# Performance work log

Hardware: AMD Instinct MI355X
Metric: run time of the kernel (lower is better)

The kernel has to match this reference:

```python
import jax, jax.numpy as jnp
import numpy as np

B, L, F, E, D, N_OUT, FC = 2048, 100, 64, 256, 256, 3, 128


def _lstm_cell(x, h, c, Wi, Wh, b):
    gates = x @ Wi + h @ Wh + b  # (B, 4H)
    i, f, g, o = jnp.split(gates, 4, axis=-1)
    c_new = jax.nn.sigmoid(f) * c + jax.nn.sigmoid(i) * jnp.tanh(g)
    h_new = jax.nn.sigmoid(o) * jnp.tanh(c_new)
    return h_new, c_new


def setup_inputs() -> dict:
    key = jax.random.key(0)
    ks = jax.random.split(key, 12)
    s = 0.05
    return {
        "x": jax.random.normal(ks[0], (B, L, F), jnp.float32),
        # encoder input-attention (shared across timesteps, as in [layer]*look_back)
        "Wa": jax.random.normal(ks[1], (F + E, F), jnp.float32) * s,
        "ba": jnp.zeros((F,), jnp.float32),
        # encoder LSTM cell
        "Wi": jax.random.normal(ks[2], (F, 4 * E), jnp.float32) * s,
        "Wh": jax.random.normal(ks[3], (E, 4 * E), jnp.float32) * s,
        "be": jnp.zeros((4 * E,), jnp.float32),
        # decoder temporal attention
        "Wd": jax.random.normal(ks[4], (E + D, D), jnp.float32) * s,
        "bd": jnp.zeros((D,), jnp.float32),
        "Wl": jax.random.normal(ks[5], (D, 1), jnp.float32) * s,
        "bl": jnp.zeros((1,), jnp.float32),
        # decoder LSTM cell
        "Wdi": jax.random.normal(ks[6], (E, 4 * D), jnp.float32) * s,
        "Wdh": jax.random.normal(ks[7], (D, 4 * D), jnp.float32) * s,
        "bdec": jnp.zeros((4 * D,), jnp.float32),
        # output head: tanh(D->FC) then tanh(FC->1)
        "Wf": jax.random.normal(ks[8], (D, FC), jnp.float32) * s,
        "bf": jnp.zeros((FC,), jnp.float32),
        "Wo": jax.random.normal(ks[9], (FC, 1), jnp.float32) * s,
        "bo": jnp.zeros((1,), jnp.float32),
    }


def reference(x, Wa, ba, Wi, Wh, be, Wd, bd, Wl, bl, Wdi, Wdh, bdec, Wf, bf, Wo, bo):
    # ---------- encoder: per-timestep input attention + LSTM cell ----------
    x_t = jnp.transpose(x, (1, 0, 2))  # (L, B, F)

    def enc_step(carry, xt):
        h, c = carry
        energies = jnp.tanh(jnp.concatenate([xt, h], axis=1) @ Wa + ba)  # (B, F)
        a = jax.nn.softmax(energies, axis=1)
        enc_in = a * xt  # attended input (B, F)
        h, c = _lstm_cell(enc_in, h, c, Wi, Wh, be)
        return (h, c), h

    h0 = jnp.zeros((B, E), x.dtype)
    c0 = jnp.zeros((B, E), x.dtype)
    _, enc_out = jax.lax.scan(enc_step, (h0, c0), x_t)  # (L, B, E)

    # ---------- decoder: temporal attention over encoder states + LSTM ----------
    h_d = jnp.zeros((B, D), x.dtype)
    c_d = jnp.zeros((B, D), x.dtype)
    outs = []
    for _ in range(N_OUT):  # small fixed output horizon
        con = jnp.broadcast_to(h_d[None, :, :], (L, B, D))
        en = jnp.tanh(jnp.concatenate([enc_out, con], axis=2) @ Wd + bd)  # (L, B, D)
        scores = en @ Wl + bl  # (L, B, 1)
        alpha = jax.nn.softmax(scores, axis=0)  # over time
        ctx = jnp.sum(alpha * enc_out, axis=0)  # (B, E)
        h_d, c_d = _lstm_cell(ctx, h_d, c_d, Wdi, Wdh, bdec)
        fc = jnp.tanh(h_d @ Wf + bf)  # (B, FC)
        outs.append(jnp.tanh(fc @ Wo + bo))  # (B, 1)
    return jnp.concatenate(outs, axis=1)  # (B, n_output)
```

## Files before the change

### kernel.cpp

```cpp
#include <hip/hip_runtime.h>
#include <math.h>

#define BB 2048
#define LL 100
#define FF 64
#define EE 256
#define DD 256
#define NOUT 3

#define COMP(v, i) ((i) == 0 ? (v).x : (i) == 1 ? (v).y : (i) == 2 ? (v).z : (v).w)

typedef unsigned short u16;
typedef unsigned int u32;
typedef __attribute__((ext_vector_type(8))) __bf16 bf16x8;
typedef __attribute__((ext_vector_type(4))) float f32x4;
typedef __attribute__((ext_vector_type(2))) float f32x2;

#define MFMA_(A, B, C) __builtin_amdgcn_mfma_f32_16x16x32_bf16((A), (B), (C), 0, 0, 0)

__device__ __forceinline__ float sigmoidf_(float x) {
    return 1.0f / (1.0f + expf(-x));
}
__device__ __forceinline__ float tanhf_(float x) {
    return 1.0f - 2.0f / (1.0f + expf(2.0f * x));
}
__device__ __forceinline__ u16 f2b_(float f) {
    u32 u = __float_as_uint(f);
    u = (u + 0x7FFFu + ((u >> 16) & 1u)) >> 16;
    return (u16)u;
}
__device__ __forceinline__ float b2f_(u16 b) {
    return __uint_as_float(((u32)b) << 16);
}
__device__ __forceinline__ u32 pack2_(float a, float b) {
    return (u32)f2b_(a) | ((u32)f2b_(b) << 16);
}
__device__ __forceinline__ f32x4 splat4(float b) {
    f32x4 v; v[0] = b; v[1] = b; v[2] = b; v[3] = b; return v;
}
__device__ __forceinline__ void split8(const float* v, uint4& H, uint4& L) {
    u16 h[8], lo[8];
    #pragma unroll
    for (int e = 0; e < 8; ++e) {
        h[e]  = f2b_(v[e]);
        lo[e] = f2b_(v[e] - b2f_(h[e]));
    }
    H = make_uint4((u32)h[0]  | ((u32)h[1]  << 16), (u32)h[2]  | ((u32)h[3]  << 16),
                   (u32)h[4]  | ((u32)h[5]  << 16), (u32)h[6]  | ((u32)h[7]  << 16));
    L = make_uint4((u32)lo[0] | ((u32)lo[1] << 16), (u32)lo[2] | ((u32)lo[3] << 16),
                   (u32)lo[4] | ((u32)lo[5] << 16), (u32)lo[6] | ((u32)lo[7] << 16));
}

#define AF(mt, kt, p, ln) (((((mt) * 10 + (kt)) * 2 + (p)) * 64 + (ln)) * 8)
#define AF2(mt, kt, p, ln) (((((mt) * 8 + (kt)) * 2 + (p)) * 64 + (ln)) * 8)

__global__ __launch_bounds__(64) void w_prep(
    const float* __restrict__ Wi, const float* __restrict__ Wh,
    const float* __restrict__ Wa, u16* __restrict__ wp)
{
    const int bid = blockIdx.x;
    const int l   = threadIdx.x;
    const int isA = (bid >= 640);
    const int b2  = isA ? bid - 640 : bid;
    const int nt  = b2 / 10, kt = b2 - nt * 10;
    const int col = nt * 16 + (l & 15);

    float v[8];
    #pragma unroll
    for (int e = 0; e < 8; ++e) {
        const int k = kt * 32 + ((l >> 4) << 3) + e;
        v[e] = isA ? Wa[(size_t)k * 64 + col]
                   : (k < 64 ? Wi[(size_t)k * 1024 + col]
                             : Wh[(size_t)(k - 64) * 1024 + col]);
    }
    uint4 H, L;
    split8(v, H, L);
    *(uint4*)&wp[(size_t)bid * 1024 + (size_t)l * 8]       = H;
    *(uint4*)&wp[(size_t)bid * 1024 + 512 + (size_t)l * 8] = L;
}

__global__ __launch_bounds__(64) void w_prep2(
    const float* __restrict__ Wd, u16* __restrict__ wp)
{
    const int bid = blockIdx.x;
    const int l   = threadIdx.x;
    const int nt  = bid >> 3, kt = bid & 7;
    const int col = nt * 16 + (l & 15);
    float v[8];
    #pragma unroll
    for (int e = 0; e < 8; ++e) {
        const int k = kt * 32 + ((l >> 4) << 3) + e;
        v[e] = Wd[(size_t)k * 256 + col];
    }
    uint4 H, L;
    split8(v, H, L);
    u16* tp = wp + (size_t)(680 + bid) * 1024;
    *(uint4*)&tp[(size_t)l * 8]       = H;
    *(uint4*)&tp[512 + (size_t)l * 8] = L;
}

__global__ __launch_bounds__(1024) void enc_mfma4(
    const float* __restrict__ x,
    const float* __restrict__ ba, const float* __restrict__ be,
    const u16* __restrict__ wp,
    float* __restrict__ enc_out,
    float* __restrict__ hbuf,
    u32* __restrict__ flags)
{
    __shared__ u16   aFrag[20480];
    __shared__ float x_s[32 * 68];
    __shared__ float e_s[32 * 68];
    __shared__ float gate_s[4][32][66];

    const int bid = blockIdx.x;
    const int g   = (bid & 7) | ((bid >> 5) << 3);
    const int p   = (bid >> 3) & 3;
    const int row0 = g * 32;
    const int tid = threadIdx.x;
    const int l   = tid & 63;
    const int w   = tid >> 6;

    for (int v = tid; v < 20480 / 2; v += 1024) ((u32*)aFrag)[v] = 0u;

    const int ntW = (w >> 2) * 16 + p * 4 + (w & 3);
    uint4 BhR[10], BlR[10];
    #pragma unroll
    for (int kt = 0; kt < 10; ++kt) {
        BhR[kt] = *(const uint4*)&wp[(size_t)(ntW * 10 + kt) * 1024 + (size_t)l * 8];
        BlR[kt] = *(const uint4*)&wp[(size_t)(ntW * 10 + kt) * 1024 + 512 + (size_t)l * 8];
    }

    const float be_r = be[(size_t)ntW * 16 + (l & 15)];
    const float ba_r = (w < 8) ? ba[(w & 3) * 16 + (l & 15)] : 0.f;

    float c_state[2] = {0.f, 0.f};

    __syncthreads();

    for (int t = 0; t < LL; ++t) {
        if (tid < 256) {
            const int kt2 = tid >> 7;
            const int mt  = (tid >> 6) & 1;
            const int l2  = tid & 63;
            const int row2 = mt * 16 + (l2 & 15);
            const int f0   = kt2 * 32 + ((l2 >> 4) << 3);
            const float* xp = x + (size_t)(row0 + row2) * (LL * FF) + (size_t)t * FF + f0;
            float4 xa = *(const float4*)xp;
            float4 xb = *(const float4*)(xp + 4);
            float v[8] = {xa.x, xa.y, xa.z, xa.w, xb.x, xb.y, xb.z, xb.w};
            uint4 H, L;
            split8(v, H, L);
            *(uint4*)&aFrag[AF(mt, kt2, 0, l2)] = H;
            *(uint4*)&aFrag[AF(mt, kt2, 1, l2)] = L;
            *(float4*)&x_s[row2 * 68 + f0]     = xa;
            *(float4*)&x_s[row2 * 68 + f0 + 4] = xb;
        } else if (t > 0) {
            const u32 target = 4u * (u32)t;
            int guard = 0;
            while (__hip_atomic_load(&flags[g * 32], __ATOMIC_RELAXED,
                                     __HIP_MEMORY_SCOPE_AGENT) < target) {
                __builtin_amdgcn_s_sleep(1);
                if (++guard > 4000000) break;
            }
            const int v   = tid - 256;
            const int prl = v >> 8;
            const int vv  = v & 255;
            const int row = vv >> 3;
            const int i8  = vv & 7;
            const int ugp = (p + 1 + prl) & 3;
            const int u8  = ugp * 64 + i8 * 8;
            const float* hp_g = hbuf + ((size_t)((t - 1) & 1) * BB + row0 + row) * 256 + u8;
            f32x4 a4, b4;
            asm volatile("global_load_dwordx4 %0, %2, off sc0 sc1\n\t"
                         "global_load_dwordx4 %1, %3, off sc0 sc1\n\t"
                         "s_waitcnt vmcnt(0)"
                         : "=v"(a4), "=v"(b4)
                         : "v"(hp_g), "v"(hp_g + 4) : "memory");
            float v8[8] = {a4[0], a4[1], a4[2], a4[3], b4[0], b4[1], b4[2], b4[3]};
            uint4 H, L;
            split8(v8, H, L);
            const int mt = row >> 4, rowT = row & 15;
            const int kt_h = 2 + (u8 >> 5);
            const int g2   = (u8 & 31) >> 3;
            const int ln   = rowT + (g2 << 4);
            *(uint4*)&aFrag[AF(mt, kt_h, 0, ln)] = H;
            *(uint4*)&aFrag[AF(mt, kt_h, 1, ln)] = L;
        }
        __syncthreads();

        if (w < 8) {
            const int mt  = w >> 2;
            const int nta = w & 3;
            f32x4 ea = splat4(ba_r);
            #pragma unroll
            for (int kt = 0; kt < 10; ++kt) {
                bf16x8 Ah = *(const bf16x8*)&aFrag[AF(mt, kt, 0, l)];
                bf16x8 Al = *(const bf16x8*)&aFrag[AF(mt, kt, 1, l)];
                const size_t o = (size_t)(640 + nta * 10 + kt) * 1024 + (size_t)l * 8;
                bf16x8 Bh = *(const bf16x8*)&wp[o];
                bf16x8 Bl = *(const bf16x8*)&wp[o + 512];
                ea = MFMA_(Ah, Bh, ea);
                ea = MFMA_(Al, Bh, ea);
                ea = MFMA_(Ah, Bl, ea);
            }
            const int colA = nta * 16 + (l & 15);
            #pragma unroll
            for (int r = 0; r < 4; ++r) {
                const int rowT = ((l >> 4) << 2) + r;
                e_s[(mt * 16 + rowT) * 68 + colA] = tanhf_(ea[r]);
            }
        }
        __syncthreads();

        if (tid < 512) {
            const int row2 = tid >> 4;
            const int c4   = (tid & 15) * 4;
            float4 ev = *(const float4*)&e_s[row2 * 68 + c4];
            float m = fmaxf(fmaxf(ev.x, ev.y), fmaxf(ev.z, ev.w));
            #pragma unroll
            for (int msk = 8; msk >= 1; msk >>= 1) m = fmaxf(m, __shfl_xor(m, msk, 64));
            float4 ex;
            ex.x = expf(ev.x - m); ex.y = expf(ev.y - m);
            ex.z = expf(ev.z - m); ex.w = expf(ev.w - m);
            float s = ex.x + ex.y + ex.z + ex.w;
            #pragma unroll
            for (int msk = 8; msk >= 1; msk >>= 1) s += __shfl_xor(s, msk, 64);
            const float inv = 1.f / s;
            float4 xv = *(const float4*)&x_s[row2 * 68 + c4];
            float ein[4] = { ex.x * inv * xv.x, ex.y * inv * xv.y,
                             ex.z * inv * xv.z, ex.w * inv * xv.w };
            const int mt   = row2 >> 4;
            const int rowT = row2 & 15;
            const int kt   = c4 >> 5;
            const int g2   = (c4 & 31) >> 3;
            const int e0   = c4 & 7;
            const int ln   = rowT + (g2 << 4);
            ushort4 h4, l4;
            #pragma unroll
            for (int e = 0; e < 4; ++e) {
                u16 hh = f2b_(ein[e]);
                u16 ll = f2b_(ein[e] - b2f_(hh));
                if (e == 0) { h4.x = hh; l4.x = ll; } else if (e == 1) { h4.y = hh; l4.y = ll; }
                else if (e == 2) { h4.z = hh; l4.z = ll; } else { h4.w = hh; l4.w = ll; }
            }
            *(ushort4*)&aFrag[AF(mt, kt, 0, ln) + e0] = h4;
            *(ushort4*)&aFrag[AF(mt, kt, 1, ln) + e0] = l4;
        }
        __syncthreads();

        f32x4 acc0 = splat4(be_r), acc1 = splat4(be_r);
        #pragma unroll
        for (int kt = 0; kt < 10; ++kt) {
            bf16x8 Ah0 = *(const bf16x8*)&aFrag[AF(0, kt, 0, l)];
            bf16x8 Al0 = *(const bf16x8*)&aFrag[AF(0, kt, 1, l)];
            bf16x8 Ah1 = *(const bf16x8*)&aFrag[AF(1, kt, 0, l)];
            bf16x8 Al1 = *(const bf16x8*)&aFrag[AF(1, kt, 1, l)];
            bf16x8 Bh  = __builtin_bit_cast(bf16x8, BhR[kt]);
            bf16x8 Bl  = __builtin_bit_cast(bf16x8, BlR[kt]);
            acc0 = MFMA_(Ah0, Bh, acc0);
            acc1 = MFMA_(Ah1, Bh, acc1);
            acc0 = MFMA_(Al0, Bh, acc0);
            acc1 = MFMA_(Al1, Bh, acc1);
            acc0 = MFMA_(Ah0, Bl, acc0);
            acc1 = MFMA_(Ah1, Bl, acc1);
        }
        {
            const int gate = w >> 2;
            const int ulb  = (w & 3) * 16 + (l & 15);
            #pragma unroll
            for (int r = 0; r < 4; ++r) {
                const int rT = ((l >> 4) << 2) + r;
                gate_s[gate][rT][ulb]      = acc0[r];
                gate_s[gate][16 + rT][ulb] = acc1[r];
            }
        }
        __syncthreads();

        {
            const int row = tid >> 5;
            const int q2  = (tid & 31) * 2;
            float gi0 = gate_s[0][row][q2], gi1 = gate_s[0][row][q2 + 1];
            float gf0 = gate_s[1][row][q2], gf1 = gate_s[1][row][q2 + 1];
            float gg0 = gate_s[2][row][q2], gg1 = gate_s[2][row][q2 + 1];
            float go0 = gate_s[3][row][q2], go1 = gate_s[3][row][q2 + 1];
            float cv0 = sigmoidf_(gf0) * c_state[0] + sigmoidf_(gi0) * tanhf_(gg0);
            float cv1 = sigmoidf_(gf1) * c_state[1] + sigmoidf_(gi1) * tanhf_(gg1);
            c_state[0] = cv0; c_state[1] = cv1;
            float hv0 = sigmoidf_(go0) * tanhf_(cv0);
            float hv1 = sigmoidf_(go1) * tanhf_(cv1);
            const int u_g = p * 64 + q2;
            *(float2*)&enc_out[((size_t)t * BB + row0 + row) * 256 + u_g]
                = make_float2(hv0, hv1);
            float* hp_g = hbuf + ((size_t)(t & 1) * BB + row0 + row) * 256 + u_g;
            f32x2 hv2; hv2[0] = hv0; hv2[1] = hv1;
            asm volatile("global_store_dwordx2 %0, %1, off sc0 sc1"
                         :: "v"(hp_g), "v"(hv2) : "memory");
            const int mt = row >> 4, rowT = row & 15;
            const int kt_h = 2 + (u_g >> 5);
            const int g2   = (u_g & 31) >> 3;
            const int ln   = rowT + (g2 << 4);
            const int e    = u_g & 7;
            ((u32*)aFrag)[(AF(mt, kt_h, 0, ln) + e) >> 1] = pack2_(hv0, hv1);
            u16 h0 = f2b_(hv0), h1 = f2b_(hv1);
            ((u32*)aFrag)[(AF(mt, kt_h, 1, ln) + e) >> 1] =
                (u32)f2b_(hv0 - b2f_(h0)) | ((u32)f2b_(hv1 - b2f_(h1)) << 16);
        }
        asm volatile("s_waitcnt vmcnt(0)" ::: "memory");
        __syncthreads();
        if (tid == 0)
            __hip_atomic_fetch_add(&flags[g * 32], 1u, __ATOMIC_RELEASE,
                                   __HIP_MEMORY_SCOPE_AGENT);
    }
}

__global__ __launch_bounds__(256) void gemm_ep_mfma(
    const float* __restrict__ A, const u16* __restrict__ wp,
    float* __restrict__ C)
{
    __shared__ u16   aF[2 * 8 * 2 * 64 * 8];
    __shared__ float c_s[32 * 260];
    const int m0  = blockIdx.x * 32;
    const int tid = threadIdx.x;
    const int l   = tid & 63;
    const int w   = tid >> 6;

    for (int s = tid; s < 1024; s += 256) {
        const int mt = s >> 9, kt = (s >> 6) & 7, l2 = s & 63;
        const int row2 = mt * 16 + (l2 & 15);
        const int k0   = kt * 32 + ((l2 >> 4) << 3);
        const float* ap = A + (size_t)(m0 + row2) * 256 + k0;
        float4 xa = *(const float4*)ap;
        float4 xb = *(const float4*)(ap + 4);
        float v[8] = {xa.x, xa.y, xa.z, xa.w, xb.x, xb.y, xb.z, xb.w};
        uint4 H, L;
        split8(v, H, L);
        *(uint4*)&aF[AF2(mt, kt, 0, l2)] = H;
        *(uint4*)&aF[AF2(mt, kt, 1, l2)] = L;
    }
    __syncthreads();

    f32x4 acc[2][4];
    #pragma unroll
    for (int mt = 0; mt < 2; ++mt)
        #pragma unroll
        for (int j = 0; j < 4; ++j) acc[mt][j] = splat4(0.f);

    #pragma unroll
    for (int kt = 0; kt < 8; ++kt) {
        bf16x8 Ah0 = *(const bf16x8*)&aF[AF2(0, kt, 0, l)];
        bf16x8 Al0 = *(const bf16x8*)&aF[AF2(0, kt, 1, l)];
        bf16x8 Ah1 = *(const bf16x8*)&aF[AF2(1, kt, 0, l)];
        bf16x8 Al1 = *(const bf16x8*)&aF[AF2(1, kt, 1, l)];
        #pragma unroll
        for (int j = 0; j < 4; ++j) {
            const int nt = w * 4 + j;
            const u16* bt = wp + (size_t)(680 + nt * 8 + kt) * 1024 + (size_t)l * 8;
            bf16x8 Bh = *(const bf16x8*)bt;
            bf16x8 Bl = *(const bf16x8*)(bt + 512);
            acc[0][j] = MFMA_(Ah0, Bh, acc[0][j]);
            acc[1][j] = MFMA_(Ah1, Bh, acc[1][j]);
            acc[0][j] = MFMA_(Al0, Bh, acc[0][j]);
            acc[1][j] = MFMA_(Al1, Bh, acc[1][j]);
            acc[0][j] = MFMA_(Ah0, Bl, acc[0][j]);
            acc[1][j] = MFMA_(Ah1, Bl, acc[1][j]);
        }
    }

    #pragma unroll
    for (int mt = 0; mt < 2; ++mt)
        #pragma unroll
        for (int j = 0; j < 4; ++j) {
            const int col = (w * 4 + j) * 16 + (l & 15);
            #pragma unroll
            for (int r = 0; r < 4; ++r) {
                const int row = mt * 16 + ((l >> 4) << 2) + r;
                c_s[row * 260 + col] = acc[mt][j][r];
            }
        }
    __syncthreads();
    for (int v = tid; v < 32 * 64; v += 256) {
        const int row = v >> 6, c4 = (v & 63) << 2;
        *(float4*)&C[(size_t)(m0 + row) * 256 + c4] = *(const float4*)&c_s[row * 260 + c4];
    }
}

__global__ __launch_bounds__(256) void gemm_nk256(
    const float* __restrict__ A, const float* __restrict__ W,
    const float* __restrict__ bias, float* __restrict__ C, int skip_gemm)
{
    __shared__ float a_s[32 * 256];
    const int m0   = blockIdx.x * 32;
    const int tid  = threadIdx.x;
    const int lane = tid & 63;
    const int rg   = tid >> 6;
    const int n0   = lane * 4;

    float4 bias4 = make_float4(0.f, 0.f, 0.f, 0.f);
    if (bias) bias4 = *(const float4*)&bias[n0];

    if (skip_gemm) {
        #pragma unroll
        for (int r = 0; r < 8; ++r)
            *(float4*)&C[(size_t)(m0 + rg * 8 + r) * 256 + n0] = bias4;
        return;
    }

    for (int v = tid; v < 32 * 64; v += 256)
        ((float4*)a_s)[v] = ((const float4*)(A + (size_t)m0 * 256))[v];
    __syncthreads();

    float4 acc[8];
    #pragma unroll
    for (int r = 0; r < 8; ++r) acc[r] = bias4;

    #pragma unroll 2
    for (int k = 0; k < 256; k += 4) {
        float4 wv[4];
        #pragma unroll
        for (int kk = 0; kk < 4; ++kk)
            wv[kk] = *(const float4*)&W[(size_t)(k + kk) * 256 + n0];
        float4 av[8];
        #pragma unroll
        for (int r = 0; r < 8; ++r)
            av[r] = *(const float4*)&a_s[(rg * 8 + r) * 256 + k];
        #pragma unroll
        for (int kk = 0; kk < 4; ++kk) {
            #pragma unroll
            for (int r = 0; r < 8; ++r) {
                float e = COMP(av[r], kk);
                acc[r].x += e * wv[kk].x; acc[r].y += e * wv[kk].y;
                acc[r].z += e * wv[kk].z; acc[r].w += e * wv[kk].w;
            }
        }
    }
    #pragma unroll
    for (int r = 0; r < 8; ++r)
        *(float4*)&C[(size_t)(m0 + rg * 8 + r) * 256 + n0] = acc[r];
}

__global__ __launch_bounds__(256) void pack_ep(
    float* A, const float* __restrict__ W, u16* epOut, int packed)
{
    __shared__ float a_s[32 * 256];
    const int m0   = blockIdx.x * 32;
    const int tid  = threadIdx.x;
    const int lane = tid & 63;
    const int rg   = tid >> 6;
    const int n0   = lane * 4;

    for (int v = tid; v < 32 * 64; v += 256)
        ((float4*)a_s)[v] = ((const float4*)(A + (size_t)m0 * 256))[v];
    __syncthreads();

    float4 acc[8];
    #pragma unroll
    for (int r = 0; r < 8; ++r) acc[r] = make_float4(0.f, 0.f, 0.f, 0.f);

    #pragma unroll 2
// ... 219 lines not shown
                acc[r].x += av.w * w3.x; acc[r].y += av.w * w3.y;
                acc[r].z += av.w * w3.z; acc[r].w += av.w * w3.w;
            }
        }
    } else if (!first) {
        const float* wP = Wdh + c0;
        #pragma unroll 2
        for (int ch = 0; ch < 64; ++ch) {
            const int k0 = ch * 4;
            float4 w0 = *(const float4*)&wP[(size_t)(k0 + 0) * 1024];
            float4 w1 = *(const float4*)&wP[(size_t)(k0 + 1) * 1024];
            float4 w2 = *(const float4*)&wP[(size_t)(k0 + 2) * 1024];
            float4 w3 = *(const float4*)&wP[(size_t)(k0 + 3) * 1024];
            #pragma unroll
            for (int r = 0; r < 8; ++r) {
                float4 av = *(const float4*)&hd_s[r * 256 + k0];
                acc[r].x += av.x * w0.x; acc[r].y += av.x * w0.y;
                acc[r].z += av.x * w0.z; acc[r].w += av.x * w0.w;
                acc[r].x += av.y * w1.x; acc[r].y += av.y * w1.y;
                acc[r].z += av.y * w1.z; acc[r].w += av.y * w1.w;
                acc[r].x += av.z * w2.x; acc[r].y += av.z * w2.y;
                acc[r].z += av.z * w2.z; acc[r].w += av.z * w2.w;
                acc[r].x += av.w * w3.x; acc[r].y += av.w * w3.y;
                acc[r].z += av.w * w3.z; acc[r].w += av.w * w3.w;
            }
        }
    }
    #pragma unroll
    for (int r = 0; r < 8; ++r)
        *(float4*)&gate_s[half][r * 1024 + c0] = acc[r];
    __syncthreads();

    {
        const float* g0 = &gate_s[0][w * 1024 + lane * 4];
        const float* g1 = &gate_s[1][w * 1024 + lane * 4];
        float4 giA = *(const float4*)&g0[0],   giB = *(const float4*)&g1[0];
        float4 gfA = *(const float4*)&g0[256], gfB = *(const float4*)&g1[256];
        float4 ggA = *(const float4*)&g0[512], ggB = *(const float4*)&g1[512];
        float4 goA = *(const float4*)&g0[768], goB = *(const float4*)&g1[768];
        size_t ci = (size_t)(row0 + w) * 256 + lane * 4;
        float4 c4 = first ? make_float4(0.f, 0.f, 0.f, 0.f)
                          : *(const float4*)&c_st[ci];
        float cc[4] = { c4.x, c4.y, c4.z, c4.w };
        float gi[4] = { giA.x + giB.x, giA.y + giB.y, giA.z + giB.z, giA.w + giB.w };
        float gf[4] = { gfA.x + gfB.x, gfA.y + gfB.y, gfA.z + gfB.z, gfA.w + gfB.w };
        float gg[4] = { ggA.x + ggB.x, ggA.y + ggB.y, ggA.z + ggB.z, ggA.w + ggB.w };
        float go[4] = { goA.x + goB.x, goA.y + goB.y, goA.z + goB.z, goA.w + goB.w };
        float4 cn, hn;
        #pragma unroll
        for (int uu = 0; uu < 4; ++uu) {
            float cv = sigmoidf_(gf[uu]) * cc[uu] + sigmoidf_(gi[uu]) * tanhf_(gg[uu]);
            float hv = sigmoidf_(go[uu]) * tanhf_(cv);
            if (uu == 0) { cn.x = cv; hn.x = hv; } else if (uu == 1) { cn.y = cv; hn.y = hv; }
            else if (uu == 2) { cn.z = cv; hn.z = hv; } else { cn.w = cv; hn.w = hv; }
        }
        *(float4*)&c_st[ci] = cn;
        *(float4*)&hd[ci]   = hn;
    }
}

__global__ __launch_bounds__(256) void head_k(
    const float* __restrict__ hd, const float* __restrict__ Wf,
    const float* __restrict__ bf, const float* __restrict__ Wo,
    const float* __restrict__ bo, float* __restrict__ out, int step)
{
    __shared__ float hd_s[16 * 256];
    __shared__ float fc_s[16 * 128];
    const int b0  = blockIdx.x * 16;
    const int tid = threadIdx.x;
    {
        const float4* hg = (const float4*)(hd + (size_t)b0 * 256);
        for (int i = tid; i < 1024; i += 256) ((float4*)hd_s)[i] = hg[i];
    }
    __syncthreads();
    {
        const int f = tid & 127, rg = tid >> 7;
        float acc[8];
        float bfv = bf[f];
        #pragma unroll
        for (int rr = 0; rr < 8; ++rr) acc[rr] = bfv;
        const float* wp = Wf + f;
        #pragma unroll 2
        for (int k = 0; k < 256; ++k) {
            float wv = wp[k * 128];
            #pragma unroll
            for (int rr = 0; rr < 8; ++rr) acc[rr] += hd_s[(rg * 8 + rr) * 256 + k] * wv;
        }
        for (int rr = 0; rr < 8; ++rr) fc_s[(rg * 8 + rr) * 128 + f] = tanhf_(acc[rr]);
    }
    __syncthreads();
    {
        const int lane = tid & 63, w = tid >> 6;
        const float bov = bo[0];
        #pragma unroll
        for (int rr = 0; rr < 4; ++rr) {
            int r = w * 4 + rr;
            float p = fc_s[r * 128 + lane] * Wo[lane] + fc_s[r * 128 + 64 + lane] * Wo[64 + lane];
            #pragma unroll
            for (int msk = 32; msk >= 1; msk >>= 1) p += __shfl_xor(p, msk, 64);
            if (lane == 0) out[(size_t)(b0 + r) * NOUT + step] = tanhf_(p + bov);
        }
    }
}

extern "C" void kernel_launch(void* const* d_in, const int* in_sizes, int n_in,
                              void* d_out, int out_size, void* d_ws, size_t ws_size,
                              hipStream_t stream)
{
    const float* x    = (const float*)d_in[0];
    const float* Wa   = (const float*)d_in[1];
    const float* ba   = (const float*)d_in[2];
    const float* Wi   = (const float*)d_in[3];
    const float* Wh   = (const float*)d_in[4];
    const float* be   = (const float*)d_in[5];
    const float* Wd   = (const float*)d_in[6];
    const float* bd   = (const float*)d_in[7];
    const float* Wl   = (const float*)d_in[8];
    const float* bl   = (const float*)d_in[9];
    const float* Wdi  = (const float*)d_in[10];
    const float* Wdh  = (const float*)d_in[11];
    const float* bdec = (const float*)d_in[12];
    const float* Wf   = (const float*)d_in[13];
    const float* bf   = (const float*)d_in[14];
    const float* Wo   = (const float*)d_in[15];
    const float* bo   = (const float*)d_in[16];
    float* out = (float*)d_out;

    const size_t f_enc    = (size_t)LL * BB * EE;
    const size_t f_state  = (size_t)BB * EE;
    const size_t f_scores = (size_t)LL * BB;
    const size_t need3 = (f_enc + 3 * f_state + f_scores) * sizeof(float);
    const size_t need2 = need3 + f_enc * sizeof(u16);
    const size_t need1 = need3 + f_enc * sizeof(float);

    float* ws      = (float*)d_ws;
    float* enc_out = ws;
    float* hd      = enc_out + f_enc;
    float* c_d     = hd + f_state;
    float* ctx     = c_d + f_state;
    float* scores  = ctx + f_state;
    float* ep32    = scores + f_scores;
    u16*   ep16    = (u16*)(scores + f_scores);
    float* hp      = ctx;
    u16*   wprep   = (u16*)ctx;
    float* hbuf    = hd;
    u32*   flags   = (u32*)scores;

    if (ws_size < need3) return;
    const int tier = (ws_size >= need1) ? 1 : (ws_size >= need2) ? 2 : 3;

    hipMemsetAsync(flags, 0, 64 * 32 * sizeof(u32), stream);
    w_prep<<<680, 64, 0, stream>>>(Wi, Wh, Wa, wprep);
    w_prep2<<<128, 64, 0, stream>>>(Wd, wprep);
    enc_mfma4<<<256, 1024, 0, stream>>>(x, ba, be, wprep, enc_out, hbuf, flags);

    if (tier == 1)
        gemm_ep_mfma<<<(LL * BB) / 32, 256, 0, stream>>>(enc_out, wprep, ep32);
    else
        pack_ep<<<(LL * BB) / 32, 256, 0, stream>>>(
            enc_out, Wd, ep16, tier == 3 ? 1 : 0);

    for (int s = 0; s < NOUT; ++s) {
        gemm_nk256<<<BB / 32, 256, 0, stream>>>(
            hd, Wd + 256 * 256, bd, hp, s == 0);
        if (tier == 1)
            scores_ep_f32<<<dim3(BB / 8, 5), 256, 0, stream>>>(ep32, hp, Wl, scores);
        else if (tier == 2)
            scores_ep_b16<<<dim3(BB / 8, 5), 256, 0, stream>>>(ep16, hp, Wl, scores, 256, 0);
        else
            scores_ep_b16<<<dim3(BB / 8, 5), 256, 0, stream>>>(
                (const u16*)enc_out, hp, Wl, scores, 512, 256);
        if (tier == 3)
            softmax_ctx_b16<<<BB / 8, 256, 0, stream>>>(scores, (const u16*)enc_out, ctx);
        else
            softmax_ctx<<<BB / 8, 256, 0, stream>>>(scores, enc_out, ctx);
        dec_step<<<BB / 8, 512, 0, stream>>>(ctx, Wdi, Wdh, bdec, hd, c_d, s == 0);
        head_k<<<BB / 16, 256, 0, stream>>>(hd, Wf, bf, Wo, bo, out, s);
    }
}
```

Baseline: 2.754 ms.

## Halve encoder block to 512 threads with two gate tiles per wave

The persistent encoder kernel drops from 1024 to 512 threads per block. Each wave now holds register-resident weights for two gate column tiles and issues twice as many MFMAs per step, and the attention GEMM has each wave cover both row tiles. Flag polling moves to a single thread followed by a barrier, and each remaining thread loads three hidden-state chunks. The LSTM elementwise stage handles four units per thread with wider stores. The aim is to cut barrier and cross-block sync cost. The trade is more register pressure, fewer waves to hide latency, and an extra barrier per timestep.

```diff
diff --git a/kernel.cpp b/kernel.cpp
--- a/kernel.cpp
+++ b/kernel.cpp
@@ -14,7 +14,6 @@
 typedef unsigned int u32;
 typedef __attribute__((ext_vector_type(8))) __bf16 bf16x8;
 typedef __attribute__((ext_vector_type(4))) float f32x4;
-typedef __attribute__((ext_vector_type(2))) float f32x2;
 
 #define MFMA_(A, B, C) __builtin_amdgcn_mfma_f32_16x16x32_bf16((A), (B), (C), 0, 0, 0)
 
@@ -99,7 +98,7 @@
     *(uint4*)&tp[512 + (size_t)l * 8] = L;
 }
 
-__global__ __launch_bounds__(1024) void enc_mfma4(
+__global__ __launch_bounds__(512, 2) void enc_mfma4(
     const float* __restrict__ x,
     const float* __restrict__ ba, const float* __restrict__ be,
     const u16* __restrict__ wp,
@@ -120,20 +119,26 @@
     const int l   = tid & 63;
     const int w   = tid >> 6;
 
-    for (int v = tid; v < 20480 / 2; v += 1024) ((u32*)aFrag)[v] = 0u;
-
-    const int ntW = (w >> 2) * 16 + p * 4 + (w & 3);
-    uint4 BhR[10], BlR[10];
+    for (int v = tid; v < 20480 / 2; v += 512) ((u32*)aFrag)[v] = 0u;
+
+    const int ln0 = 2 * w, ln1 = 2 * w + 1;
+    const int ntW0 = (ln0 >> 2) * 16 + p * 4 + (ln0 & 3);
+    const int ntW1 = (ln1 >> 2) * 16 + p * 4 + (ln1 & 3);
+    uint4 BH0[10], BL0[10], BH1[10], BL1[10];
     #pragma unroll
     for (int kt = 0; kt < 10; ++kt) {
-        BhR[kt] = *(const uint4*)&wp[(size_t)(ntW * 10 + kt) * 1024 + (size_t)l * 8];
-        BlR[kt] = *(const uint4*)&wp[(size_t)(ntW * 10 + kt) * 1024 + 512 + (size_t)l * 8];
-    }
-
-    const float be_r = be[(size_t)ntW * 16 + (l & 15)];
-    const float ba_r = (w < 8) ? ba[(w & 3) * 16 + (l & 15)] : 0.f;
-
-    float c_state[2] = {0.f, 0.f};
+        const size_t o0 = (size_t)(ntW0 * 10 + kt) * 1024 + (size_t)l * 8;
+        const size_t o1 = (size_t)(ntW1 * 10 + kt) * 1024 + (size_t)l * 8;
+        BH0[kt] = *(const uint4*)&wp[o0];
+        BL0[kt] = *(const uint4*)&wp[o0 + 512];
+        BH1[kt] = *(const uint4*)&wp[o1];
+        BL1[kt] = *(const uint4*)&wp[o1 + 512];
+    }
+    const float be_r0 = be[(size_t)ntW0 * 16 + (l & 15)];
+    const float be_r1 = be[(size_t)ntW1 * 16 + (l & 15)];
+    const float ba_r  = (w < 4) ? ba[w * 16 + (l & 15)] : 0.f;
+
+    float c_state[4] = {0.f, 0.f, 0.f, 0.f};
 
     __syncthreads();
 
@@ -154,65 +159,86 @@
             *(uint4*)&aFrag[AF(mt, kt2, 1, l2)] = L;
             *(float4*)&x_s[row2 * 68 + f0]     = xa;
             *(float4*)&x_s[row2 * 68 + f0 + 4] = xb;
-        } else if (t > 0) {
+        } else if (tid == 511 && t > 0) {
             const u32 target = 4u * (u32)t;
             int guard = 0;
             while (__hip_atomic_load(&flags[g * 32], __ATOMIC_RELAXED,
                                      __HIP_MEMORY_SCOPE_AGENT) < target) {
                 __builtin_amdgcn_s_sleep(1);
-                if (++guard > 4000000) break;
-            }
-            const int v   = tid - 256;
-            const int prl = v >> 8;
-            const int vv  = v & 255;
-            const int row = vv >> 3;
-            const int i8  = vv & 7;
-            const int ugp = (p + 1 + prl) & 3;
-            const int u8  = ugp * 64 + i8 * 8;
-            const float* hp_g = hbuf + ((size_t)((t - 1) & 1) * BB + row0 + row) * 256 + u8;
-            f32x4 a4, b4;
-            asm volatile("global_load_dwordx4 %0, %2, off sc0 sc1\n\t"
-                         "global_load_dwordx4 %1, %3, off sc0 sc1\n\t"
-                         "s_waitcnt vmcnt(0)"
-                         : "=v"(a4), "=v"(b4)
-                         : "v"(hp_g), "v"(hp_g + 4) : "memory");
-            float v8[8] = {a4[0], a4[1], a4[2], a4[3], b4[0], b4[1], b4[2], b4[3]};
-            uint4 H, L;
-            split8(v8, H, L);
+                if (++guard > 2000000) break;
+            }
+        }
+        __syncthreads();
+
+        if (t > 0 && tid >= 256) {
+            const int base = tid - 256;
+            const int row  = base >> 3;
+            const int i8   = base & 7;
+            const float* hb = hbuf + ((size_t)((t - 1) & 1) * BB + row0 + row) * 256;
+            const int u8a = (((p + 1) & 3) * 64) + i8 * 8;
+            const int u8b = (((p + 2) & 3) * 64) + i8 * 8;
+            const int u8c = (((p + 3) & 3) * 64) + i8 * 8;
+            f32x4 d0, d1, d2, d3, d4, d5;
+            asm volatile(
+                "global_load_dwordx4 %0, %6, off sc0 sc1\n\t"
+                "global_load_dwordx4 %1, %7, off sc0 sc1\n\t"
+                "global_load_dwordx4 %2, %8, off sc0 sc1\n\t"
+                "global_load_dwordx4 %3, %9, off sc0 sc1\n\t"
+                "global_load_dwordx4 %4, %10, off sc0 sc1\n\t"
+                "global_load_dwordx4 %5, %11, off sc0 sc1\n\t"
+                "s_waitcnt vmcnt(0)"
+                : "=v"(d0), "=v"(d1), "=v"(d2), "=v"(d3), "=v"(d4), "=v"(d5)
+                : "v"(hb + u8a), "v"(hb + u8a + 4),
+                  "v"(hb + u8b), "v"(hb + u8b + 4),
+                  "v"(hb + u8c), "v"(hb + u8c + 4)
+                : "memory");
             const int mt = row >> 4, rowT = row & 15;
-            const int kt_h = 2 + (u8 >> 5);
-            const int g2   = (u8 & 31) >> 3;
-            const int ln   = rowT + (g2 << 4);
-            *(uint4*)&aFrag[AF(mt, kt_h, 0, ln)] = H;
-            *(uint4*)&aFrag[AF(mt, kt_h, 1, ln)] = L;
+            #pragma unroll
+            for (int it = 0; it < 3; ++it) {
+                const int u8 = (it == 0) ? u8a : (it == 1) ? u8b : u8c;
+                f32x4 A4 = (it == 0) ? d0 : (it == 1) ? d2 : d4;
+                f32x4 B4 = (it == 0) ? d1 : (it == 1) ? d3 : d5;
+                float v8[8] = {A4[0], A4[1], A4[2], A4[3], B4[0], B4[1], B4[2], B4[3]};
+                uint4 H, L;
+                split8(v8, H, L);
+                const int kt_h = 2 + (u8 >> 5);
+                const int g2   = (u8 & 31) >> 3;
+                const int lnA  = rowT + (g2 << 4);
+                *(uint4*)&aFrag[AF(mt, kt_h, 0, lnA)] = H;
+                *(uint4*)&aFrag[AF(mt, kt_h, 1, lnA)] = L;
+            }
         }
         __syncthreads();
 
-        if (w < 8) {
-            const int mt  = w >> 2;
-            const int nta = w & 3;
-            f32x4 ea = splat4(ba_r);
+        if (w < 4) {
+            f32x4 ea0 = splat4(ba_r), ea1 = splat4(ba_r);
             #pragma unroll
             for (int kt = 0; kt < 10; ++kt) {
-                bf16x8 Ah = *(const bf16x8*)&aFrag[AF(mt, kt, 0, l)];
-                bf16x8 Al = *(const bf16x8*)&aFrag[AF(mt, kt, 1, l)];
-                const size_t o = (size_t)(640 + nta * 10 + kt) * 1024 + (size_t)l * 8;
+                bf16x8 Ah0 = *(const bf16x8*)&aFrag[AF(0, kt, 0, l)];
+                bf16x8 Al0 = *(const bf16x8*)&aFrag[AF(0, kt, 1, l)];
+                bf16x8 Ah1 = *(const bf16x8*)&aFrag[AF(1, kt, 0, l)];
+                bf16x8 Al1 = *(const bf16x8*)&aFrag[AF(1, kt, 1, l)];
+                const size_t o = (size_t)(640 + w * 10 + kt) * 1024 + (size_t)l * 8;
                 bf16x8 Bh = *(const bf16x8*)&wp[o];
                 bf16x8 Bl = *(const bf16x8*)&wp[o + 512];
-                ea = MFMA_(Ah, Bh, ea);
-                ea = MFMA_(Al, Bh, ea);
-                ea = MFMA_(Ah, Bl, ea);
-            }
-            const int colA = nta * 16 + (l & 15);
+                ea0 = MFMA_(Ah0, Bh, ea0);
+                ea1 = MFMA_(Ah1, Bh, ea1);
+                ea0 = MFMA_(Al0, Bh, ea0);
+                ea1 = MFMA_(Al1, Bh, ea1);
+                ea0 = MFMA_(Ah0, Bl, ea0);
+                ea1 = MFMA_(Ah1, Bl, ea1);
+            }
+            const int colA = w * 16 + (l & 15);
             #pragma unroll
             for (int r = 0; r < 4; ++r) {
                 const int rowT = ((l >> 4) << 2) + r;
-                e_s[(mt * 16 + rowT) * 68 + colA] = tanhf_(ea[r]);
+                e_s[(rowT)      * 68 + colA] = tanhf_(ea0[r]);
+                e_s[(16 + rowT) * 68 + colA] = tanhf_(ea1[r]);
             }
         }
         __syncthreads();
 
-        if (tid < 512) {
+        {
             const int row2 = tid >> 4;
             const int c4   = (tid & 15) * 4;
             float4 ev = *(const float4*)&e_s[row2 * 68 + c4];
@@ -234,7 +260,7 @@
             const int kt   = c4 >> 5;
             const int g2   = (c4 & 31) >> 3;
             const int e0   = c4 & 7;
-            const int ln   = rowT + (g2 << 4);
+            const int lnA  = rowT + (g2 << 4);
             ushort4 h4, l4;
             #pragma unroll
             for (int e = 0; e < 4; ++e) {
@@ -243,67 +269,77 @@
                 if (e == 0) { h4.x = hh; l4.x = ll; } else if (e == 1) { h4.y = hh; l4.y = ll; }
                 else if (e == 2) { h4.z = hh; l4.z = ll; } else { h4.w = hh; l4.w = ll; }
             }
-            *(ushort4*)&aFrag[AF(mt, kt, 0, ln) + e0] = h4;
-            *(ushort4*)&aFrag[AF(mt, kt, 1, ln) + e0] = l4;
+            *(ushort4*)&aFrag[AF(mt, kt, 0, lnA) + e0] = h4;
+            *(ushort4*)&aFrag[AF(mt, kt, 1, lnA) + e0] = l4;
         }
         __syncthreads();
 
-        f32x4 acc0 = splat4(be_r), acc1 = splat4(be_r);
+        f32x4 a00 = splat4(be_r0), a10 = splat4(be_r0);
+        f32x4 a01 = splat4(be_r1), a11 = splat4(be_r1);
         #pragma unroll
         for (int kt = 0; kt < 10; ++kt) {
             bf16x8 Ah0 = *(const bf16x8*)&aFrag[AF(0, kt, 0, l)];
             bf16x8 Al0 = *(const bf16x8*)&aFrag[AF(0, kt, 1, l)];
             bf16x8 Ah1 = *(const bf16x8*)&aFrag[AF(1, kt, 0, l)];
             bf16x8 Al1 = *(const bf16x8*)&aFrag[AF(1, kt, 1, l)];
-            bf16x8 Bh  = __builtin_bit_cast(bf16x8, BhR[kt]);
-            bf16x8 Bl  = __builtin_bit_cast(bf16x8, BlR[kt]);
-            acc0 = MFMA_(Ah0, Bh, acc0);
-            acc1 = MFMA_(Ah1, Bh, acc1);
-            acc0 = MFMA_(Al0, Bh, acc0);
-            acc1 = MFMA_(Al1, Bh, acc1);
-            acc0 = MFMA_(Ah0, Bl, acc0);
-            acc1 = MFMA_(Ah1, Bl, acc1);
+            bf16x8 bh0 = __builtin_bit_cast(bf16x8, BH0[kt]);
+            bf16x8 bl0 = __builtin_bit_cast(bf16x8, BL0[kt]);
+            bf16x8 bh1 = __builtin_bit_cast(bf16x8, BH1[kt]);
+            bf16x8 bl1 = __builtin_bit_cast(bf16x8, BL1[kt]);
+            a00 = MFMA_(Ah0, bh0, a00);  a01 = MFMA_(Ah0, bh1, a01);
+            a10 = MFMA_(Ah1, bh0, a10);  a11 = MFMA_(Ah1, bh1, a11);
+            a00 = MFMA_(Al0, bh0, a00);  a01 = MFMA_(Al0, bh1, a01);
+            a10 = MFMA_(Al1, bh0, a10);  a11 = MFMA_(Al1, bh1, a11);
+            a00 = MFMA_(Ah0, bl0, a00);  a01 = MFMA_(Ah0, bl1, a01);
+            a10 = MFMA_(Ah1, bl0, a10);  a11 = MFMA_(Ah1, bl1, a11);
         }
         {
-            const int gate = w >> 2;
-            const int ulb  = (w & 3) * 16 + (l & 15);
+            const int ga0 = ln0 >> 2, ulb0 = (ln0 & 3) * 16 + (l & 15);
+            const int ga1 = ln1 >> 2, ulb1 = (ln1 & 3) * 16 + (l & 15);
             #pragma unroll
             for (int r = 0; r < 4; ++r) {
                 const int rT = ((l >> 4) << 2) + r;
-                gate_s[gate][rT][ulb]      = acc0[r];
-                gate_s[gate][16 + rT][ulb] = acc1[r];
+                gate_s[ga0][rT][ulb0]      = a00[r];
+                gate_s[ga0][16 + rT][ulb0] = a10[r];
+                gate_s[ga1][rT][ulb1]      = a01[r];
+                gate_s[ga1][16 + rT][ulb1] = a11[r];
             }
         }
         __syncthreads();
 
         {
-            const int row = tid >> 5;
-            const int q2  = (tid & 31) * 2;
-            float gi0 = gate_s[0][row][q2], gi1 = gate_s[0][row][q2 + 1];
-            float gf0 = gate_s[1][row][q2], gf1 = gate_s[1][row][q2 + 1];
-            float gg0 = gate_s[2][row][q2], gg1 = gate_s[2][row][q2 + 1];
-            float go0 = gate_s[3][row][q2], go1 = gate_s[3][row][q2 + 1];
-            float cv0 = sigmoidf_(gf0) * c_state[0] + sigmoidf_(gi0) * tanhf_(gg0);
-            float cv1 = sigmoidf_(gf1) * c_state[1] + sigmoidf_(gi1) * tanhf_(gg1);
-            c_state[0] = cv0; c_state[1] = cv1;
-            float hv0 = sigmoidf_(go0) * tanhf_(cv0);
-            float hv1 = sigmoidf_(go1) * tanhf_(cv1);
-            const int u_g = p * 64 + q2;
-            *(float2*)&enc_out[((size_t)t * BB + row0 + row) * 256 + u_g]
-                = make_float2(hv0, hv1);
+            const int row = tid >> 4;
+            const int q4  = (tid & 15) * 4;
+            float hv[4];
+            #pragma unroll
+            for (int j = 0; j < 4; ++j) {
+                const float gi = gate_s[0][row][q4 + j];
+                const float gf = gate_s[1][row][q4 + j];
+                const float gg = gate_s[2][row][q4 + j];
+                const float go = gate_s[3][row][q4 + j];
+                const float cv = sigmoidf_(gf) * c_state[j] + sigmoidf_(gi) * tanhf_(gg);
+                c_state[j] = cv;
+                hv[j] = sigmoidf_(go) * tanhf_(cv);
+            }
+            const int u_g = p * 64 + q4;
+            float4 h4 = make_float4(hv[0], hv[1], hv[2], hv[3]);
+            *(float4*)&enc_out[((size_t)t * BB + row0 + row) * 256 + u_g] = h4;
             float* hp_g = hbuf + ((size_t)(t & 1) * BB + row0 + row) * 256 + u_g;
-            f32x2 hv2; hv2[0] = hv0; hv2[1] = hv1;
-            asm volatile("global_store_dwordx2 %0, %1, off sc0 sc1"
-                         :: "v"(hp_g), "v"(hv2) : "memory");
+            f32x4 hvv; hvv[0] = hv[0]; hvv[1] = hv[1]; hvv[2] = hv[2]; hvv[3] = hv[3];
+            asm volatile("global_store_dwordx4 %0, %1, off sc0 sc1"
+                         :: "v"(hp_g), "v"(hvv) : "memory");
             const int mt = row >> 4, rowT = row & 15;
             const int kt_h = 2 + (u_g >> 5);
             const int g2   = (u_g & 31) >> 3;
-            const int ln   = rowT + (g2 << 4);
+            const int lnA  = rowT + (g2 << 4);
             const int e    = u_g & 7;
-            ((u32*)aFrag)[(AF(mt, kt_h, 0, ln) + e) >> 1] = pack2_(hv0, hv1);
-            u16 h0 = f2b_(hv0), h1 = f2b_(hv1);
-            ((u32*)aFrag)[(AF(mt, kt_h, 1, ln) + e) >> 1] =
-                (u32)f2b_(hv0 - b2f_(h0)) | ((u32)f2b_(hv1 - b2f_(h1)) << 16);
+            ushort4 hh, ll;
+            hh.x = f2b_(hv[0]); ll.x = f2b_(hv[0] - b2f_(hh.x));
+            hh.y = f2b_(hv[1]); ll.y = f2b_(hv[1] - b2f_(hh.y));
+            hh.z = f2b_(hv[2]); ll.z = f2b_(hv[2] - b2f_(hh.z));
+            hh.w = f2b_(hv[3]); ll.w = f2b_(hv[3] - b2f_(hh.w));
+            *(ushort4*)&aFrag[AF(mt, kt_h, 0, lnA) + e] = hh;
+            *(ushort4*)&aFrag[AF(mt, kt_h, 1, lnA) + e] = ll;
         }
         asm volatile("s_waitcnt vmcnt(0)" ::: "memory");
         __syncthreads();
@@ -829,7 +865,7 @@
     hipMemsetAsync(flags, 0, 64 * 32 * sizeof(u32), stream);
     w_prep<<<680, 64, 0, stream>>>(Wi, Wh, Wa, wprep);
     w_prep2<<<128, 64, 0, stream>>>(Wd, wprep);
-    enc_mfma4<<<256, 1024, 0, stream>>>(x, ba, be, wprep, enc_out, hbuf, flags);
+    enc_mfma4<<<256, 512, 0, stream>>>(x, ba, be, wprep, enc_out, hbuf, flags);
 
     if (tier == 1)
         gemm_ep_mfma<<<(LL * BB) / 32, 256, 0, stream>>>(enc_out, wprep, ep32);
```

After: 2.470 ms. -10.3%, faster.

## Swizzle LDS A-fragments, single-thread flag spin, stream low weight halves from global

Applied to the files above, without the earlier changes.

Applies an XOR swizzle to the lane index of the shared A-fragment layout so that fragment reads and writes hit fewer LDS bank conflicts. The cross-block flag wait now uses a single spinning thread followed by a block barrier, instead of 768 threads polling, which cuts atomic traffic to the flag. The per-thread register copy of the low-half weight fragments is dropped and reloaded from global memory on every step, freeing registers at the cost of extra loads. Gate reads are vectorised to float2, and the spin-guard limit is halved.

```diff
diff --git a/kernel.cpp b/kernel.cpp
--- a/kernel.cpp
+++ b/kernel.cpp
@@ -52,6 +52,7 @@
 }
 
 #define AF(mt, kt, p, ln) (((((mt) * 10 + (kt)) * 2 + (p)) * 64 + (ln)) * 8)
+#define AFX(mt, kt, p, ln) AF(mt, kt, p, (ln) ^ (((ln) >> 4) & 3))
 #define AF2(mt, kt, p, ln) (((((mt) * 8 + (kt)) * 2 + (p)) * 64 + (ln)) * 8)
 
 __global__ __launch_bounds__(64) void w_prep(
@@ -123,12 +124,10 @@
     for (int v = tid; v < 20480 / 2; v += 1024) ((u32*)aFrag)[v] = 0u;
 
     const int ntW = (w >> 2) * 16 + p * 4 + (w & 3);
-    uint4 BhR[10], BlR[10];
-    #pragma unroll
-    for (int kt = 0; kt < 10; ++kt) {
+    uint4 BhR[10];
+    #pragma unroll
+    for (int kt = 0; kt < 10; ++kt)
         BhR[kt] = *(const uint4*)&wp[(size_t)(ntW * 10 + kt) * 1024 + (size_t)l * 8];
-        BlR[kt] = *(const uint4*)&wp[(size_t)(ntW * 10 + kt) * 1024 + 512 + (size_t)l * 8];
-    }
 
     const float be_r = be[(size_t)ntW * 16 + (l & 15)];
     const float ba_r = (w < 8) ? ba[(w & 3) * 16 + (l & 15)] : 0.f;
@@ -150,18 +149,22 @@
             float v[8] = {xa.x, xa.y, xa.z, xa.w, xb.x, xb.y, xb.z, xb.w};
             uint4 H, L;
             split8(v, H, L);
-            *(uint4*)&aFrag[AF(mt, kt2, 0, l2)] = H;
-            *(uint4*)&aFrag[AF(mt, kt2, 1, l2)] = L;
+            *(uint4*)&aFrag[AFX(mt, kt2, 0, l2)] = H;
+            *(uint4*)&aFrag[AFX(mt, kt2, 1, l2)] = L;
             *(float4*)&x_s[row2 * 68 + f0]     = xa;
             *(float4*)&x_s[row2 * 68 + f0 + 4] = xb;
-        } else if (t > 0) {
+        } else if (tid == 1023 && t > 0) {
             const u32 target = 4u * (u32)t;
             int guard = 0;
             while (__hip_atomic_load(&flags[g * 32], __ATOMIC_RELAXED,
                                      __HIP_MEMORY_SCOPE_AGENT) < target) {
                 __builtin_amdgcn_s_sleep(1);
-                if (++guard > 4000000) break;
-            }
+                if (++guard > 2000000) break;
+            }
+        }
+        __syncthreads();
+
+        if (t > 0 && tid >= 256) {
             const int v   = tid - 256;
             const int prl = v >> 8;
             const int vv  = v & 255;
@@ -183,8 +186,8 @@
             const int kt_h = 2 + (u8 >> 5);
             const int g2   = (u8 & 31) >> 3;
             const int ln   = rowT + (g2 << 4);
-            *(uint4*)&aFrag[AF(mt, kt_h, 0, ln)] = H;
-            *(uint4*)&aFrag[AF(mt, kt_h, 1, ln)] = L;
+            *(uint4*)&aFrag[AFX(mt, kt_h, 0, ln)] = H;
+            *(uint4*)&aFrag[AFX(mt, kt_h, 1, ln)] = L;
         }
         __syncthreads();
 
@@ -194,8 +197,8 @@
             f32x4 ea = splat4(ba_r);
             #pragma unroll
             for (int kt = 0; kt < 10; ++kt) {
-                bf16x8 Ah = *(const bf16x8*)&aFrag[AF(mt, kt, 0, l)];
-                bf16x8 Al = *(const bf16x8*)&aFrag[AF(mt, kt, 1, l)];
+                bf16x8 Ah = *(const bf16x8*)&aFrag[AFX(mt, kt, 0, l)];
+                bf16x8 Al = *(const bf16x8*)&aFrag[AFX(mt, kt, 1, l)];
                 const size_t o = (size_t)(640 + nta * 10 + kt) * 1024 + (size_t)l * 8;
                 bf16x8 Bh = *(const bf16x8*)&wp[o];
                 bf16x8 Bl = *(const bf16x8*)&wp[o + 512];
@@ -243,20 +246,20 @@
                 if (e == 0) { h4.x = hh; l4.x = ll; } else if (e == 1) { h4.y = hh; l4.y = ll; }
                 else if (e == 2) { h4.z = hh; l4.z = ll; } else { h4.w = hh; l4.w = ll; }
             }
-            *(ushort4*)&aFrag[AF(mt, kt, 0, ln) + e0] = h4;
-            *(ushort4*)&aFrag[AF(mt, kt, 1, ln) + e0] = l4;
+            *(ushort4*)&aFrag[AFX(mt, kt, 0, ln) + e0] = h4;
+            *(ushort4*)&aFrag[AFX(mt, kt, 1, ln) + e0] = l4;
         }
         __syncthreads();
 
         f32x4 acc0 = splat4(be_r), acc1 = splat4(be_r);
         #pragma unroll
         for (int kt = 0; kt < 10; ++kt) {
-            bf16x8 Ah0 = *(const bf16x8*)&aFrag[AF(0, kt, 0, l)];
-            bf16x8 Al0 = *(const bf16x8*)&aFrag[AF(0, kt, 1, l)];
-            bf16x8 Ah1 = *(const bf16x8*)&aFrag[AF(1, kt, 0, l)];
-            bf16x8 Al1 = *(const bf16x8*)&aFrag[AF(1, kt, 1, l)];
+            bf16x8 Ah0 = *(const bf16x8*)&aFrag[AFX(0, kt, 0, l)];
+            bf16x8 Al0 = *(const bf16x8*)&aFrag[AFX(0, kt, 1, l)];
+            bf16x8 Ah1 = *(const bf16x8*)&aFrag[AFX(1, kt, 0, l)];
+            bf16x8 Al1 = *(const bf16x8*)&aFrag[AFX(1, kt, 1, l)];
+            bf16x8 Bl  = *(const bf16x8*)&wp[(size_t)(ntW * 10 + kt) * 1024 + 512 + (size_t)l * 8];
             bf16x8 Bh  = __builtin_bit_cast(bf16x8, BhR[kt]);
-            bf16x8 Bl  = __builtin_bit_cast(bf16x8, BlR[kt]);
             acc0 = MFMA_(Ah0, Bh, acc0);
             acc1 = MFMA_(Ah1, Bh, acc1);
             acc0 = MFMA_(Al0, Bh, acc0);
@@ -279,15 +282,15 @@
         {
             const int row = tid >> 5;
             const int q2  = (tid & 31) * 2;
-            float gi0 = gate_s[0][row][q2], gi1 = gate_s[0][row][q2 + 1];
-            float gf0 = gate_s[1][row][q2], gf1 = gate_s[1][row][q2 + 1];
-            float gg0 = gate_s[2][row][q2], gg1 = gate_s[2][row][q2 + 1];
-            float go0 = gate_s[3][row][q2], go1 = gate_s[3][row][q2 + 1];
-            float cv0 = sigmoidf_(gf0) * c_state[0] + sigmoidf_(gi0) * tanhf_(gg0);
-            float cv1 = sigmoidf_(gf1) * c_state[1] + sigmoidf_(gi1) * tanhf_(gg1);
+            float2 gi2 = *(const float2*)&gate_s[0][row][q2];
+            float2 gf2 = *(const float2*)&gate_s[1][row][q2];
+            float2 gg2 = *(const float2*)&gate_s[2][row][q2];
+            float2 go2 = *(const float2*)&gate_s[3][row][q2];
+            float cv0 = sigmoidf_(gf2.x) * c_state[0] + sigmoidf_(gi2.x) * tanhf_(gg2.x);
+            float cv1 = sigmoidf_(gf2.y) * c_state[1] + sigmoidf_(gi2.y) * tanhf_(gg2.y);
             c_state[0] = cv0; c_state[1] = cv1;
-            float hv0 = sigmoidf_(go0) * tanhf_(cv0);
-            float hv1 = sigmoidf_(go1) * tanhf_(cv1);
+            float hv0 = sigmoidf_(go2.x) * tanhf_(cv0);
+            float hv1 = sigmoidf_(go2.y) * tanhf_(cv1);
             const int u_g = p * 64 + q2;
             *(float2*)&enc_out[((size_t)t * BB + row0 + row) * 256 + u_g]
                 = make_float2(hv0, hv1);
@@ -300,9 +303,9 @@
             const int g2   = (u_g & 31) >> 3;
             const int ln   = rowT + (g2 << 4);
             const int e    = u_g & 7;
-            ((u32*)aFrag)[(AF(mt, kt_h, 0, ln) + e) >> 1] = pack2_(hv0, hv1);
+            ((u32*)aFrag)[(AFX(mt, kt_h, 0, ln) + e) >> 1] = pack2_(hv0, hv1);
             u16 h0 = f2b_(hv0), h1 = f2b_(hv1);
-            ((u32*)aFrag)[(AF(mt, kt_h, 1, ln) + e) >> 1] =
+            ((u32*)aFrag)[(AFX(mt, kt_h, 1, ln) + e) >> 1] =
                 (u32)f2b_(hv0 - b2f_(h0)) | ((u32)f2b_(hv1 - b2f_(h1)) << 16);
         }
         asm volatile("s_waitcnt vmcnt(0)" ::: "memory");
```

Measured after the change: 2.481 ms. -9.9%, faster.
